# Optimization experiments

Measured on AMD Instinct MI355X. Metric: run time of the kernel, lower is better.

## Reference

```python
import jax, jax.numpy as jnp
import numpy as np
import math

B, Q, CQ = 2, 2048, 512
H, D = 8, 64  # no_heads, c_hidden

def setup_inputs() -> dict:
    key = jax.random.key(0)
    ks = jax.random.split(key, 8)
    s = 0.02
    return {
        "q_x": jax.random.normal(ks[0], (B, Q, CQ), jnp.float32),
        "kv_x": jax.random.normal(ks[1], (B, Q, CQ), jnp.float32),
        "bias": jax.random.normal(ks[2], (B, 1, Q, Q), jnp.float32),
        "w_qkv": jax.random.normal(ks[3], (3 * H * D, CQ), jnp.float32) * s,
        "w_o": jax.random.normal(ks[4], (CQ, H * D), jnp.float32) * s,
        "b_o": jnp.zeros((CQ,), jnp.float32),
        "w_g": jax.random.normal(ks[5], (H * D, CQ), jnp.float32) * s,
        "b_g": jnp.zeros((H * D,), jnp.float32),
    }

def reference(q_x, kv_x, bias, w_qkv, w_o, b_o, w_g, b_g):
    # Fused QKV projection from q_x (kv_x is unused by the original module's _prep_qkv)
    qkv = jnp.einsum('bqc,ec->bqe', q_x, w_qkv)  # [B,Q,3*H*D]
    q, k, v = jnp.split(qkv, 3, axis=-1)
    q = q.reshape(B, Q, H, D) / math.sqrt(D)
    k = k.reshape(B, Q, H, D)
    v = v.reshape(B, Q, H, D)
    # scores + additive pairwise bias, softmax over keys
    scores = jnp.einsum('bqhd,bkhd->bhqk', q, k) + bias  # [B,H,Q,K]
    attn = jax.nn.softmax(scores, axis=-1)
    o = jnp.einsum('bhqk,bkhd->bqhd', attn, v)  # [B,Q,H,D]
    # sigmoid gating
    g = jax.nn.sigmoid(jnp.einsum('bqc,ec->bqe', q_x, w_g) + b_g).reshape(B, Q, H, D)
    o = o * g
    # output projection
    o = o.reshape(B, Q, H * D)
    return jnp.einsum('bqe,ce->bqc', o, w_o) + b_o
```

## Files before the change

kernel.cpp:

```cpp
#include <hip/hip_runtime.h>
#include <math.h>

#define B_  2
#define Q_  2048
#define CQ_ 512
#define H_  8
#define D_  64
#define M_  (B_*Q_)
#define L2E 1.44269504088896f

typedef __bf16 bf16;
typedef __bf16 bf16x4 __attribute__((ext_vector_type(4)));
typedef __bf16 bf16x8 __attribute__((ext_vector_type(8)));
typedef float  f32x4  __attribute__((ext_vector_type(4)));
typedef float  f32x16 __attribute__((ext_vector_type(16)));

__device__ __forceinline__ void gl_lds16(const bf16* g, bf16* l) {
    __builtin_amdgcn_global_load_lds(
        (const __attribute__((address_space(1))) unsigned int*)g,
        (__attribute__((address_space(3))) unsigned int*)l, 16, 0, 0);
}

#define S0 (4096*512)
#define S1 (1536*512)
#define S2 (512*512)
#define S3 (512*512)
__global__ __launch_bounds__(256)
void convert_kernel(const float* __restrict__ qx, const float* __restrict__ wqkv,
                    const float* __restrict__ wg, const float* __restrict__ wo,
                    bf16* __restrict__ qxb, bf16* __restrict__ wcat, bf16* __restrict__ wob)
{
    const long long t = (long long)blockIdx.x * 256 + threadIdx.x;
    const long long e = t * 8;
    const float* src; bf16* dst;
    if (e < S0)                { src = qx + e;                  dst = qxb + e; }
    else if (e < S0 + S1)      { src = wqkv + (e - S0);         dst = wcat + (e - S0); }
    else if (e < S0 + S1 + S2) { src = wg + (e - S0 - S1);      dst = wcat + S1 + (e - S0 - S1); }
    else                       { src = wo + (e - S0 - S1 - S2); dst = wob + (e - S0 - S1 - S2); }
    const float4 a = *(const float4*)(src);
    const float4 b = *(const float4*)(src + 4);
    bf16x8 v;
    v[0] = (bf16)a.x; v[1] = (bf16)a.y; v[2] = (bf16)a.z; v[3] = (bf16)a.w;
    v[4] = (bf16)b.x; v[5] = (bf16)b.y; v[6] = (bf16)b.z; v[7] = (bf16)b.w;
    *(bf16x8*)dst = v;
}

template<int BM, int BN, int EPI>
__global__ __launch_bounds__(256)
void gemm_bf16(const bf16* __restrict__ A, const bf16* __restrict__ W,
               const float* __restrict__ bvec, float* __restrict__ fout,
               bf16* __restrict__ qb, bf16* __restrict__ kb, bf16* __restrict__ vb,
               bf16* __restrict__ gb)
{
    constexpr int MI = BM / 32, NJ = BN / 32;
    __shared__ __align__(16) bf16 As[BM * 32];
    __shared__ __align__(16) bf16 Bs[BN * 32];

    const int t = threadIdx.x;
    const int w = t >> 6, lane = t & 63;
    const int l15 = lane & 15, quad = lane >> 4;
    const int wm = w & 1, wn = w >> 1;
    const int bm = blockIdx.x * BM;
    const int bn = blockIdx.y * BN;

    f32x4 acc[MI][NJ] = {};

    const int rr = t >> 2;
    const int cc = (t & 3) * 8;

    for (int k0 = 0; k0 < 512; k0 += 32) {
        #pragma unroll
        for (int i = 0; i < BM / 64; ++i)
            gl_lds16(A + (size_t)(bm + i * 64 + rr) * 512 + k0 + cc,
                     As + (i * 64 + w * 16) * 32);
        #pragma unroll
        for (int i = 0; i < BN / 64; ++i)
            gl_lds16(W + (size_t)(bn + i * 64 + rr) * 512 + k0 + cc,
                     Bs + (i * 64 + w * 16) * 32);
        __asm__ volatile("s_waitcnt vmcnt(0)" ::: "memory");
        __syncthreads();

        bf16x8 af[MI], bfr[NJ];
        #pragma unroll
        for (int i = 0; i < MI; ++i)
            af[i] = *(const bf16x8*)(As + (wm * (BM / 2) + i * 16 + l15) * 32 + quad * 8);
        #pragma unroll
        for (int j = 0; j < NJ; ++j)
            bfr[j] = *(const bf16x8*)(Bs + (wn * (BN / 2) + j * 16 + l15) * 32 + quad * 8);
        #pragma unroll
        for (int i = 0; i < MI; ++i)
            #pragma unroll
            for (int j = 0; j < NJ; ++j)
                acc[i][j] = __builtin_amdgcn_mfma_f32_16x16x32_bf16(af[i], bfr[j], acc[i][j], 0, 0, 0);
        __syncthreads();
    }

    #pragma unroll
    for (int i = 0; i < MI; ++i) {
        #pragma unroll
        for (int r = 0; r < 4; ++r) {
            const int m = bm + wm * (BM / 2) + i * 16 + quad * 4 + r;
            const int b = m >> 11, qq = m & 2047;
            #pragma unroll
            for (int j = 0; j < NJ; ++j) {
                const int n = bn + wn * (BN / 2) + j * 16 + l15;
                const float cval = acc[i][j][r];
                if constexpr (EPI == 0) {
                    const int part = n >> 9;
                    const int h = (n >> 6) & 7, d = n & 63;
                    const size_t bhbase = (size_t)(b * H_ + h) * (Q_ * D_);
                    if (part == 0) {
                        qb[bhbase + (size_t)qq * D_ + d] = (bf16)(cval * (0.125f * L2E));
                    } else if (part == 1) {
                        kb[bhbase + (qq >> 6) * 4096 + ((qq >> 5) & 1) * 2048
                           + (d >> 4) * 512 + ((d >> 3) & 1) * 256
                           + (qq & 31) * 8 + (d & 7)] = (bf16)cval;
                    } else if (part == 2) {
                        vb[bhbase + (qq >> 6) * 4096 + (d >> 5) * 2048
                           + ((qq & 63) >> 4) * 512 + ((qq >> 3) & 1) * 256
                           + (d & 31) * 8 + (qq & 7)] = (bf16)cval;
                    } else {
                        const int gcol = n & 511;
                        const float x = cval + bvec[gcol];
                        gb[(size_t)m * 512 + gcol] = (bf16)(1.f / (1.f + __expf(-x)));
                    }
                } else {
                    fout[(size_t)m * 512 + n] = cval + bvec[n];
                }
            }
        }
    }
}

__global__ __launch_bounds__(256, 1)
void attn_kernel(const bf16* __restrict__ qb, const bf16* __restrict__ kf,
                 const bf16* __restrict__ vf, const float* __restrict__ bias,
                 const bf16* __restrict__ g, bf16* __restrict__ og)
{
    __shared__ __align__(16) bf16 Ks[2][4096];
    __shared__ __align__(16) bf16 Vs[2][4096];
    __shared__ __align__(16) bf16 Ps[4][32 * 72];

    const int tid  = threadIdx.x;
    const int wv   = tid >> 6, lane = tid & 63;
    const int l31  = lane & 31, b5 = lane >> 5;
    const int x    = blockIdx.x;
    const int bh   = ((x & 7) << 1) | (x >> 3);
    const int b    = bh >> 3, h = bh & 7;
    const int qg   = blockIdx.y * 128 + wv * 32 + l31;

    const bf16* qp = qb + ((size_t)bh * Q_ + qg) * D_;
    bf16x8 bq[4];
    #pragma unroll
    for (int c = 0; c < 4; ++c)
        bq[c] = *(const bf16x8*)(qp + c * 16 + b5 * 8);

    f32x16 acc[2] = {};
    float m_run = -INFINITY, l_run = 0.f;

    const bf16*  kfb  = kf + (size_t)bh * (Q_ * D_);
    const bf16*  vfb  = vf + (size_t)bh * (Q_ * D_);
    const float* brow = bias + ((size_t)b * Q_ + qg) * Q_;

    f32x4 bcur[8], bnxt[8];

    #pragma unroll
    for (int p = 0; p < 2; ++p) {
        gl_lds16(kfb + (wv * 2 + p) * 512 + lane * 8, Ks[0] + (wv * 2 + p) * 512);
        gl_lds16(vfb + (wv * 2 + p) * 512 + lane * 8, Vs[0] + (wv * 2 + p) * 512);
    }
    #pragma unroll
    for (int i = 0; i < 8; ++i)
        bcur[i] = *(const f32x4*)(brow + (i >> 2) * 32 + (i & 3) * 8 + b5 * 4);
    __asm__ volatile("s_waitcnt vmcnt(0)" ::: "memory");
    __syncthreads();

    bf16* pw = Ps[wv] + l31 * 72;

    int cur = 0;
    #pragma unroll 1
    for (int t = 0; t < 32; ++t) {
        if (t < 31) {
            const size_t off = (size_t)(t + 1) * 4096;
            #pragma unroll
            for (int p = 0; p < 2; ++p) {
                gl_lds16(kfb + off + (wv * 2 + p) * 512 + lane * 8,
                         Ks[cur ^ 1] + (wv * 2 + p) * 512);
                gl_lds16(vfb + off + (wv * 2 + p) * 512 + lane * 8,
                         Vs[cur ^ 1] + (wv * 2 + p) * 512);
            }
            const int k0n = (t + 1) * 64;
            #pragma unroll
            for (int i = 0; i < 8; ++i)
                bnxt[i] = *(const f32x4*)(brow + k0n + (i >> 2) * 32 + (i & 3) * 8 + b5 * 4);
        }

        const bf16* Kc = Ks[cur];
        f32x16 sv[2] = {};
        #pragma unroll
        for (int kg = 0; kg < 2; ++kg)
            #pragma unroll
            for (int c = 0; c < 4; ++c) {
                const bf16x8 ak = *(const bf16x8*)(Kc + kg * 2048 + c * 512 + lane * 8);
                sv[kg] = __builtin_amdgcn_mfma_f32_32x32x16_bf16(ak, bq[c], sv[kg], 0, 0, 0);
            }

        float sc[2][16];
        #pragma unroll
        for (int kg = 0; kg < 2; ++kg)
            #pragma unroll
            for (int r = 0; r < 16; ++r)
                sc[kg][r] = fmaf(bcur[kg * 4 + (r >> 2)][r & 3], L2E, sv[kg][r]);

        float tmax = -INFINITY;
        #pragma unroll
        for (int kg = 0; kg < 2; ++kg)
            #pragma unroll
            for (int r = 0; r < 16; ++r)
                tmax = fmaxf(tmax, sc[kg][r]);
        tmax = fmaxf(tmax, __shfl_xor(tmax, 32, 64));

        const float mn = fmaxf(m_run, tmax);
        const float alpha = __builtin_amdgcn_exp2f(m_run - mn);
        m_run = mn;

        float rsum = 0.f;
        #pragma unroll
        for (int kg = 0; kg < 2; ++kg)
            #pragma unroll
            for (int r = 0; r < 16; ++r) {
                sc[kg][r] = __builtin_amdgcn_exp2f(sc[kg][r] - mn);
                rsum += sc[kg][r];
            }
        rsum += __shfl_xor(rsum, 32, 64);
        l_run = l_run * alpha + rsum;
        acc[0] *= alpha;
        acc[1] *= alpha;

        #pragma unroll
        for (int kg = 0; kg < 2; ++kg)
            #pragma unroll
            for (int gi = 0; gi < 4; ++gi) {
                bf16x4 p4;
                p4[0] = (bf16)sc[kg][gi * 4 + 0];
                p4[1] = (bf16)sc[kg][gi * 4 + 1];
                p4[2] = (bf16)sc[kg][gi * 4 + 2];
                p4[3] = (bf16)sc[kg][gi * 4 + 3];
                *(bf16x4*)(pw + kg * 32 + gi * 8 + b5 * 4) = p4;
            }
        __asm__ volatile("s_waitcnt lgkmcnt(0)" ::: "memory");

        const bf16* Vc = Vs[cur];
        #pragma unroll
        for (int c4 = 0; c4 < 4; ++c4) {
            const bf16x8 bp = *(const bf16x8*)(pw + c4 * 16 + b5 * 8);
            #pragma unroll
            for (int dg = 0; dg < 2; ++dg) {
                const bf16x8 av = *(const bf16x8*)(Vc + dg * 2048 + c4 * 512 + lane * 8);
                acc[dg] = __builtin_amdgcn_mfma_f32_32x32x16_bf16(av, bp, acc[dg], 0, 0, 0);
            }
        }

        if (t < 31) {
            #pragma unroll
            for (int i = 0; i < 8; ++i) bcur[i] = bnxt[i];
        }
        __asm__ volatile("s_waitcnt vmcnt(0)" ::: "memory");
        __syncthreads();
        cur ^= 1;
    }

    const float inv = 1.f / l_run;
    const size_t obase = ((size_t)(b * Q_ + qg)) * 512 + h * 64;
    #pragma unroll
    for (int dg = 0; dg < 2; ++dg)
        #pragma unroll
        for (int gi = 0; gi < 4; ++gi) {
            const int d0 = dg * 32 + gi * 8 + b5 * 4;
            const bf16x4 gv = *(const bf16x4*)(g + obase + d0);
            bf16x4 ov;
            #pragma unroll
            for (int r = 0; r < 4; ++r)
                ov[r] = (bf16)(acc[dg][gi * 4 + r] * inv * (float)gv[r]);
            *(bf16x4*)(og + obase + d0) = ov;
        }
}

extern "C" void kernel_launch(void* const* d_in, const int* in_sizes, int n_in,
                              void* d_out, int out_size, void* d_ws, size_t ws_size,
                              hipStream_t stream)
{
    const float* q_x   = (const float*)d_in[0];
    const float* bias  = (const float*)d_in[2];
    const float* w_qkv = (const float*)d_in[3];
    const float* w_o   = (const float*)d_in[4];
    const float* b_o   = (const float*)d_in[5];
    const float* w_g   = (const float*)d_in[6];
    const float* b_g   = (const float*)d_in[7];
    float* out = (float*)d_out;

    char* ws = (char*)d_ws;
    bf16* qxb  = (bf16*)(ws);
    bf16* wcat = (bf16*)(ws + (4u  << 20));
    bf16* wob  = (bf16*)(ws + (6u  << 20));
    bf16* qb   = (bf16*)(ws + (8u  << 20));
    bf16* kb   = (bf16*)(ws + (12u << 20));
    bf16* vb   = (bf16*)(ws + (16u << 20));
    bf16* gb   = (bf16*)(ws + (20u << 20));
    bf16* ogb  = (bf16*)(ws + (24u << 20));

    convert_kernel<<<(S0 + S1 + S2 + S3) / (256 * 8), 256, 0, stream>>>(
        q_x, w_qkv, w_g, w_o, qxb, wcat, wob);
    gemm_bf16<128, 128, 0><<<dim3(32, 16), 256, 0, stream>>>(
        qxb, wcat, b_g, nullptr, qb, kb, vb, gb);
    attn_kernel<<<dim3(B_ * H_, Q_ / 128), 256, 0, stream>>>(qb, kb, vb, bias, gb, ogb);
    gemm_bf16<64, 128, 1><<<dim3(64, 4), 256, 0, stream>>>(
        ogb, wob, b_o, out, nullptr, nullptr, nullptr, nullptr);
}
```

Before: 214.6 us.

## Split attention over key halves with merge kernel; vectorize GEMM epilogue stores

Attention now runs as a split-K (flash-decoding style) pass: each block handles half of the keys, writes a normalized partial output plus running max/sum, and a new merge kernel combines the two halves and applies the sigmoid gate. This doubles the grid from 256 to 512 blocks, and the launch bound allows 3 blocks per CU, to improve occupancy on a GPU with many CUs. The cost is an extra launch and partial-output traffic. Separately, the QKV/output GEMM swaps MFMA operands for most tiles so each lane holds 4 contiguous columns and can issue vectorized bf16x4/float4 stores instead of scalar stores.

```diff
diff --git a/kernel.cpp b/kernel.cpp
--- a/kernel.cpp
+++ b/kernel.cpp
@@ -62,6 +62,7 @@
     const int wm = w & 1, wn = w >> 1;
     const int bm = blockIdx.x * BM;
     const int bn = blockIdx.y * BN;
+    const bool swapped = (EPI == 1) || ((bn >> 9) != 2);
 
     f32x4 acc[MI][NJ] = {};
 
@@ -87,55 +88,95 @@
         #pragma unroll
         for (int j = 0; j < NJ; ++j)
             bfr[j] = *(const bf16x8*)(Bs + (wn * (BN / 2) + j * 16 + l15) * 32 + quad * 8);
-        #pragma unroll
-        for (int i = 0; i < MI; ++i)
-            #pragma unroll
-            for (int j = 0; j < NJ; ++j)
-                acc[i][j] = __builtin_amdgcn_mfma_f32_16x16x32_bf16(af[i], bfr[j], acc[i][j], 0, 0, 0);
+        if (swapped) {
+            #pragma unroll
+            for (int i = 0; i < MI; ++i)
+                #pragma unroll
+                for (int j = 0; j < NJ; ++j)
+                    acc[i][j] = __builtin_amdgcn_mfma_f32_16x16x32_bf16(bfr[j], af[i], acc[i][j], 0, 0, 0);
+        } else {
+            #pragma unroll
+            for (int i = 0; i < MI; ++i)
+                #pragma unroll
+                for (int j = 0; j < NJ; ++j)
+                    acc[i][j] = __builtin_amdgcn_mfma_f32_16x16x32_bf16(af[i], bfr[j], acc[i][j], 0, 0, 0);
+        }
         __syncthreads();
     }
 
-    #pragma unroll
-    for (int i = 0; i < MI; ++i) {
-        #pragma unroll
-        for (int r = 0; r < 4; ++r) {
-            const int m = bm + wm * (BM / 2) + i * 16 + quad * 4 + r;
+    if (swapped) {
+        #pragma unroll
+        for (int i = 0; i < MI; ++i) {
+            const int m = bm + wm * (BM / 2) + i * 16 + l15;
             const int b = m >> 11, qq = m & 2047;
+            #pragma unroll
+            for (int j = 0; j < NJ; ++j) {
+                const int n0 = bn + wn * (BN / 2) + j * 16 + quad * 4;
+                const f32x4 cv = acc[i][j];
+                if constexpr (EPI == 1) {
+                    float4 st;
+                    st.x = cv[0] + bvec[n0 + 0];
+                    st.y = cv[1] + bvec[n0 + 1];
+                    st.z = cv[2] + bvec[n0 + 2];
+                    st.w = cv[3] + bvec[n0 + 3];
+                    *(float4*)(fout + (size_t)m * 512 + n0) = st;
+                } else {
+                    const int part = n0 >> 9;
+                    if (part == 0) {
+                        const int h = (n0 >> 6) & 7, d0 = n0 & 63;
+                        bf16x4 q4;
+                        #pragma unroll
+                        for (int r = 0; r < 4; ++r) q4[r] = (bf16)(cv[r] * (0.125f * L2E));
+                        *(bf16x4*)(qb + (size_t)(b * H_ + h) * (Q_ * D_) + (size_t)qq * 64 + d0) = q4;
+                    } else if (part == 1) {
+                        const int h = (n0 >> 6) & 7, d0 = n0 & 63;
+                        const size_t off = (size_t)(b * H_ + h) * (Q_ * D_)
+                            + (qq >> 6) * 4096 + ((qq >> 5) & 1) * 2048
+                            + (d0 >> 4) * 512 + ((d0 >> 3) & 1) * 256
+                            + (qq & 31) * 8 + (d0 & 7);
+                        bf16x4 k4;
+                        #pragma unroll
+                        for (int r = 0; r < 4; ++r) k4[r] = (bf16)cv[r];
+                        *(bf16x4*)(kb + off) = k4;
+                    } else {
+                        const int gcol = n0 & 511;
+                        const float4 bv4 = *(const float4*)(bvec + gcol);
+                        bf16x4 g4;
+                        g4[0] = (bf16)(1.f / (1.f + __expf(-(cv[0] + bv4.x))));
+                        g4[1] = (bf16)(1.f / (1.f + __expf(-(cv[1] + bv4.y))));
+                        g4[2] = (bf16)(1.f / (1.f + __expf(-(cv[2] + bv4.z))));
+                        g4[3] = (bf16)(1.f / (1.f + __expf(-(cv[3] + bv4.w))));
+                        *(bf16x4*)(gb + (size_t)m * 512 + gcol) = g4;
+                    }
+                }
+            }
+        }
+    } else {
+        #pragma unroll
+        for (int i = 0; i < MI; ++i) {
+            const int m0 = bm + wm * (BM / 2) + i * 16 + quad * 4;
+            const int b = m0 >> 11, qq0 = m0 & 2047;
             #pragma unroll
             for (int j = 0; j < NJ; ++j) {
                 const int n = bn + wn * (BN / 2) + j * 16 + l15;
-                const float cval = acc[i][j][r];
-                if constexpr (EPI == 0) {
-                    const int part = n >> 9;
-                    const int h = (n >> 6) & 7, d = n & 63;
-                    const size_t bhbase = (size_t)(b * H_ + h) * (Q_ * D_);
-                    if (part == 0) {
-                        qb[bhbase + (size_t)qq * D_ + d] = (bf16)(cval * (0.125f * L2E));
-                    } else if (part == 1) {
-                        kb[bhbase + (qq >> 6) * 4096 + ((qq >> 5) & 1) * 2048
-                           + (d >> 4) * 512 + ((d >> 3) & 1) * 256
-                           + (qq & 31) * 8 + (d & 7)] = (bf16)cval;
-                    } else if (part == 2) {
-                        vb[bhbase + (qq >> 6) * 4096 + (d >> 5) * 2048
-                           + ((qq & 63) >> 4) * 512 + ((qq >> 3) & 1) * 256
-                           + (d & 31) * 8 + (qq & 7)] = (bf16)cval;
-                    } else {
-                        const int gcol = n & 511;
-                        const float x = cval + bvec[gcol];
-                        gb[(size_t)m * 512 + gcol] = (bf16)(1.f / (1.f + __expf(-x)));
-                    }
-                } else {
-                    fout[(size_t)m * 512 + n] = cval + bvec[n];
-                }
+                const int h = (n >> 6) & 7, d = n & 63;
+                const size_t off = (size_t)(b * H_ + h) * (Q_ * D_)
+                    + (qq0 >> 6) * 4096 + (d >> 5) * 2048
+                    + ((qq0 & 63) >> 4) * 512 + ((qq0 >> 3) & 1) * 256
+                    + (d & 31) * 8 + (qq0 & 7);
+                bf16x4 v4;
+                #pragma unroll
+                for (int r = 0; r < 4; ++r) v4[r] = (bf16)acc[i][j][r];
+                *(bf16x4*)(vb + off) = v4;
             }
         }
     }
 }
 
-__global__ __launch_bounds__(256, 1)
-void attn_kernel(const bf16* __restrict__ qb, const bf16* __restrict__ kf,
-                 const bf16* __restrict__ vf, const float* __restrict__ bias,
-                 const bf16* __restrict__ g, bf16* __restrict__ og)
+__global__ __launch_bounds__(256, 3)
+void attn_part(const bf16* __restrict__ qb, const bf16* __restrict__ kf,
+               const bf16* __restrict__ vf, const float* __restrict__ bias,
+               bf16* __restrict__ po, float2* __restrict__ ml)
 {
     __shared__ __align__(16) bf16 Ks[2][4096];
     __shared__ __align__(16) bf16 Vs[2][4096];
@@ -146,8 +187,9 @@
     const int l31  = lane & 31, b5 = lane >> 5;
     const int x    = blockIdx.x;
     const int bh   = ((x & 7) << 1) | (x >> 3);
-    const int b    = bh >> 3, h = bh & 7;
+    const int b    = bh >> 3;
     const int qg   = blockIdx.y * 128 + wv * 32 + l31;
+    const int ks   = blockIdx.z;
 
     const bf16* qp = qb + ((size_t)bh * Q_ + qg) * D_;
     bf16x8 bq[4];
@@ -158,9 +200,9 @@
     f32x16 acc[2] = {};
     float m_run = -INFINITY, l_run = 0.f;
 
-    const bf16*  kfb  = kf + (size_t)bh * (Q_ * D_);
-    const bf16*  vfb  = vf + (size_t)bh * (Q_ * D_);
-    const float* brow = bias + ((size_t)b * Q_ + qg) * Q_;
+    const bf16*  kfb  = kf + (size_t)bh * (Q_ * D_) + (size_t)ks * 16 * 4096;
+    const bf16*  vfb  = vf + (size_t)bh * (Q_ * D_) + (size_t)ks * 16 * 4096;
+    const float* brow = bias + ((size_t)b * Q_ + qg) * Q_ + ks * 1024;
 
     f32x4 bcur[8], bnxt[8];
 
@@ -179,8 +221,8 @@
 
     int cur = 0;
     #pragma unroll 1
-    for (int t = 0; t < 32; ++t) {
-        if (t < 31) {
+    for (int t = 0; t < 16; ++t) {
+        if (t < 15) {
             const size_t off = (size_t)(t + 1) * 4096;
             #pragma unroll
             for (int p = 0; p < 2; ++p) {
@@ -261,7 +303,7 @@
             }
         }
 
-        if (t < 31) {
+        if (t < 15) {
             #pragma unroll
             for (int i = 0; i < 8; ++i) bcur[i] = bnxt[i];
         }
@@ -271,19 +313,49 @@
     }
 
     const float inv = 1.f / l_run;
-    const size_t obase = ((size_t)(b * Q_ + qg)) * 512 + h * 64;
+    const size_t pbase = ((size_t)(ks * 16 + bh) * Q_ + qg) * 64;
     #pragma unroll
     for (int dg = 0; dg < 2; ++dg)
         #pragma unroll
         for (int gi = 0; gi < 4; ++gi) {
             const int d0 = dg * 32 + gi * 8 + b5 * 4;
-            const bf16x4 gv = *(const bf16x4*)(g + obase + d0);
             bf16x4 ov;
             #pragma unroll
             for (int r = 0; r < 4; ++r)
-                ov[r] = (bf16)(acc[dg][gi * 4 + r] * inv * (float)gv[r]);
-            *(bf16x4*)(og + obase + d0) = ov;
-        }
+                ov[r] = (bf16)(acc[dg][gi * 4 + r] * inv);
+            *(bf16x4*)(po + pbase + d0) = ov;
+        }
+    if (b5 == 0)
+        ml[(size_t)(ks * 16 + bh) * Q_ + qg] = make_float2(m_run, l_run);
+}
+
+__global__ __launch_bounds__(256)
+void merge_kernel(const bf16* __restrict__ po, const float2* __restrict__ ml,
+                  const bf16* __restrict__ g, bf16* __restrict__ og)
+{
+    const int gid = blockIdx.x * 256 + threadIdx.x;
+    const int row = gid >> 3;
+    const int d8  = (gid & 7) * 8;
+    const int bh  = row >> 11, qg = row & 2047;
+    const int b   = bh >> 3, h = bh & 7;
+
+    const float2 ml0 = ml[row];
+    const float2 ml1 = ml[16 * Q_ + row];
+    const float  M   = fmaxf(ml0.x, ml1.x);
+    const float  w0r = ml0.y * __builtin_amdgcn_exp2f(ml0.x - M);
+    const float  w1r = ml1.y * __builtin_amdgcn_exp2f(ml1.x - M);
+    const float  inv = 1.f / (w0r + w1r);
+    const float  w0 = w0r * inv, w1 = w1r * inv;
+
+    const bf16x8 o0 = *(const bf16x8*)(po + (size_t)row * 64 + d8);
+    const bf16x8 o1 = *(const bf16x8*)(po + (size_t)16 * Q_ * 64 + (size_t)row * 64 + d8);
+    const size_t obase = ((size_t)(b * Q_ + qg)) * 512 + h * 64 + d8;
+    const bf16x8 gv = *(const bf16x8*)(g + obase);
+    bf16x8 ov;
+    #pragma unroll
+    for (int r = 0; r < 8; ++r)
+        ov[r] = (bf16)(((float)o0[r] * w0 + (float)o1[r] * w1) * (float)gv[r]);
+    *(bf16x8*)(og + obase) = ov;
 }
 
 extern "C" void kernel_launch(void* const* d_in, const int* in_sizes, int n_in,
@@ -300,20 +372,23 @@
     float* out = (float*)d_out;
 
     char* ws = (char*)d_ws;
-    bf16* qxb  = (bf16*)(ws);
-    bf16* wcat = (bf16*)(ws + (4u  << 20));
-    bf16* wob  = (bf16*)(ws + (6u  << 20));
-    bf16* qb   = (bf16*)(ws + (8u  << 20));
-    bf16* kb   = (bf16*)(ws + (12u << 20));
-    bf16* vb   = (bf16*)(ws + (16u << 20));
-    bf16* gb   = (bf16*)(ws + (20u << 20));
-    bf16* ogb  = (bf16*)(ws + (24u << 20));
+    bf16*   qxb  = (bf16*)(ws);
+    bf16*   wcat = (bf16*)(ws + (4u  << 20));
+    bf16*   po   = (bf16*)(ws);
+    bf16*   qb   = (bf16*)(ws + (8u  << 20));
+    bf16*   kb   = (bf16*)(ws + (12u << 20));
+    bf16*   vb   = (bf16*)(ws + (16u << 20));
+    bf16*   gb   = (bf16*)(ws + (20u << 20));
+    bf16*   ogb  = (bf16*)(ws + (24u << 20));
+    bf16*   wob  = (bf16*)(ws + (28u << 20));
+    float2* ml   = (float2*)(ws + (28u << 20) + (1u << 19));
 
     convert_kernel<<<(S0 + S1 + S2 + S3) / (256 * 8), 256, 0, stream>>>(
         q_x, w_qkv, w_g, w_o, qxb, wcat, wob);
     gemm_bf16<128, 128, 0><<<dim3(32, 16), 256, 0, stream>>>(
         qxb, wcat, b_g, nullptr, qb, kb, vb, gb);
-    attn_kernel<<<dim3(B_ * H_, Q_ / 128), 256, 0, stream>>>(qb, kb, vb, bias, gb, ogb);
+    attn_part<<<dim3(B_ * H_, Q_ / 128, 2), 256, 0, stream>>>(qb, kb, vb, bias, po, ml);
+    merge_kernel<<<(16 * Q_ * 8) / 256, 256, 0, stream>>>(po, ml, gb, ogb);
     gemm_bf16<64, 128, 1><<<dim3(64, 4), 256, 0, stream>>>(
         ogb, wob, b_o, out, nullptr, nullptr, nullptr, nullptr);
 }
```

After: 180.3 us. 1.19x faster.
